# Kernel optimization log

Measured on AMD Instinct MI355X. Metric: run time of the kernel, lower is better.

The kernel has to match this reference:

```python
import jax, jax.numpy as jnp
import numpy as np

B, N, EMB, H, DH = 1, 196, 256, 8, 32
HID = 4 * EMB
EPS = 1e-5
SCALE = 16.0  # emb_size ** 0.5 (torch code scales by emb_size, not head_dim)


def _ln(x, w, b):
    m = jnp.mean(x, axis=-1, keepdims=True)
    v = jnp.mean((x - m) ** 2, axis=-1, keepdims=True)
    return (x - m) * jax.lax.rsqrt(v + EPS) * w + b


def _qkv(x, W, bias):
    # rearrange 'b n (h d qkv) -> qkv b h n d'
    t = (x @ W + bias).reshape(B, N, H, DH, 3)
    t = jnp.transpose(t, (4, 0, 2, 1, 3))
    return t[0], t[1], t[2]


def _attn(q, k, v, Wp, bp):
    att = jax.nn.softmax(jnp.einsum('bhqd,bhkd->bhqk', q, k) / SCALE, axis=-1)
    o = jnp.einsum('bhqk,bhkd->bhqd', att, v)
    o = jnp.transpose(o, (0, 2, 1, 3)).reshape(B, N, EMB)  # b n (h d)
    return o @ Wp + bp


def _ff(x, W1, b1, W2, b2):
    return jax.nn.gelu(x @ W1 + b1, approximate=False) @ W2 + b2


def _recon(x):
    x = x.reshape(B, 14, 14, 16, 16)
    x = jnp.transpose(x, (0, 3, 4, 1, 2))
    return x.reshape(B, 1, 224, 224)


def setup_inputs() -> dict:
    key = jax.random.key(0)
    ks = jax.random.split(key, 16)
    rn = lambda k, shape: jax.random.normal(k, shape, jnp.float32) * 0.02
    d = {
        'vis_emb': jax.random.normal(ks[0], (B, N, EMB), jnp.float32),
        'ir_emb': jax.random.normal(ks[1], (B, N, EMB), jnp.float32),
        'ln1v_w': jnp.ones((EMB,), jnp.float32), 'ln1v_b': jnp.zeros((EMB,), jnp.float32),
        'ln1i_w': jnp.ones((EMB,), jnp.float32), 'ln1i_b': jnp.zeros((EMB,), jnp.float32),
        'ln2v_w': jnp.ones((EMB,), jnp.float32), 'ln2v_b': jnp.zeros((EMB,), jnp.float32),
        'ln2i_w': jnp.ones((EMB,), jnp.float32), 'ln2i_b': jnp.zeros((EMB,), jnp.float32),
        'Wqkv_v': rn(ks[2], (EMB, 3 * EMB)), 'bqkv_v': jnp.zeros((3 * EMB,), jnp.float32),
        'Wqkv_i': rn(ks[3], (EMB, 3 * EMB)), 'bqkv_i': jnp.zeros((3 * EMB,), jnp.float32),
        'Wp_v': rn(ks[4], (EMB, EMB)), 'bp_v': jnp.zeros((EMB,), jnp.float32),
        'Wp_i': rn(ks[5], (EMB, EMB)), 'bp_i': jnp.zeros((EMB,), jnp.float32),
        'W1v': rn(ks[6], (EMB, HID)), 'b1v': jnp.zeros((HID,), jnp.float32),
        'W2v': rn(ks[7], (HID, EMB)), 'b2v': jnp.zeros((EMB,), jnp.float32),
        'W1i': rn(ks[8], (EMB, HID)), 'b1i': jnp.zeros((HID,), jnp.float32),
        'W2i': rn(ks[9], (HID, EMB)), 'b2i': jnp.zeros((EMB,), jnp.float32),
    }
    return d


def reference(vis_emb, ir_emb, ln1v_w, ln1v_b, ln1i_w, ln1i_b, ln2v_w, ln2v_b,
              ln2i_w, ln2i_b, Wqkv_v, bqkv_v, Wqkv_i, bqkv_i, Wp_v, bp_v,
              Wp_i, bp_i, W1v, b1v, W2v, b2v, W1i, b1i, W2i, b2i):
    nv = _ln(vis_emb, ln1v_w, ln1v_b)
    ni = _ln(ir_emb, ln1i_w, ln1i_b)
    qv, kv_, vv = _qkv(vis_emb, Wqkv_v, bqkv_v)
    qi, ki, vi = _qkv(ir_emb, Wqkv_i, bqkv_i)
    cross_v2i = _attn(qv, ki, vi, Wp_v, bp_v)   # vis queries attend ir k/v
    cross_i2v = _attn(qi, kv_, vv, Wp_i, bp_i)  # ir queries attend vis k/v
    rv = nv + cross_v2i
    ri = ni + cross_i2v
    lv = _ln(rv, ln2v_w, ln2v_b)
    li = _ln(ri, ln2i_w, ln2i_b)
    ov = _ff(lv, W1v, b1v, W2v, b2v) + lv
    oi = _ff(li, W1i, b1i, W2i, b2i) + li
    return jnp.concatenate([_recon(oi), _recon(ov)], axis=1)  # (1,2,224,224)
```

## Files before the change

kernel.cpp:

```cpp
#include <hip/hip_runtime.h>
#include <math.h>

#define NT   196
#define EMB  256
#define NH   8
#define DH   32
#define HID  1024
#define EPSV 1e-5f


__global__ __launch_bounds__(256) void k1_qkv(
    const float* __restrict__ vis, const float* __restrict__ ir,
    const float* __restrict__ Wqkv_v, const float* __restrict__ bqkv_v,
    const float* __restrict__ Wqkv_i, const float* __restrict__ bqkv_i,
    float* __restrict__ Q, float* __restrict__ Kq, float* __restrict__ Vq)
{
    const int b = blockIdx.x;
    const int s = b / 147;
    const int rem = b % 147;
    const int mt = rem / 3;
    const int cg = rem % 3;
    const int n0 = mt * 4;
    const int t = threadIdx.x;

    const float* x    = (s == 0) ? vis    : ir;
    const float* W    = (s == 0) ? Wqkv_v : Wqkv_i;
    const float* bias = (s == 0) ? bqkv_v : bqkv_i;

    __shared__ float xsT[EMB * 4];
    __shared__ float pp[4 * 4 * 256];

    {
        int r = t >> 6, c4 = (t & 63) * 4;
        float4 xv = *(const float4*)&x[(n0 + r) * EMB + c4];
        xsT[(c4 + 0) * 4 + r] = xv.x;
        xsT[(c4 + 1) * 4 + r] = xv.y;
        xsT[(c4 + 2) * 4 + r] = xv.z;
        xsT[(c4 + 3) * 4 + r] = xv.w;
    }
    __syncthreads();

    const int cq = t & 63, ks = t >> 6;
    const int col0 = cg * 256 + cq * 4;
    const float* Wb = W + col0;
    float4 a0 = {0,0,0,0}, a1 = a0, a2 = a0, a3 = a0;
    #pragma unroll 8
    for (int kk = ks * 64; kk < ks * 64 + 64; kk++) {
        float4 w4 = *(const float4*)&Wb[kk * 768];
        float4 xr = *(const float4*)&xsT[kk * 4];
        a0.x = fmaf(xr.x, w4.x, a0.x); a0.y = fmaf(xr.x, w4.y, a0.y);
        a0.z = fmaf(xr.x, w4.z, a0.z); a0.w = fmaf(xr.x, w4.w, a0.w);
        a1.x = fmaf(xr.y, w4.x, a1.x); a1.y = fmaf(xr.y, w4.y, a1.y);
        a1.z = fmaf(xr.y, w4.z, a1.z); a1.w = fmaf(xr.y, w4.w, a1.w);
        a2.x = fmaf(xr.z, w4.x, a2.x); a2.y = fmaf(xr.z, w4.y, a2.y);
        a2.z = fmaf(xr.z, w4.z, a2.z); a2.w = fmaf(xr.z, w4.w, a2.w);
        a3.x = fmaf(xr.w, w4.x, a3.x); a3.y = fmaf(xr.w, w4.y, a3.y);
        a3.z = fmaf(xr.w, w4.z, a3.z); a3.w = fmaf(xr.w, w4.w, a3.w);
    }
    *(float4*)&pp[(ks * 4 + 0) * 256 + cq * 4] = a0;
    *(float4*)&pp[(ks * 4 + 1) * 256 + cq * 4] = a1;
    *(float4*)&pp[(ks * 4 + 2) * 256 + cq * 4] = a2;
    *(float4*)&pp[(ks * 4 + 3) * 256 + cq * 4] = a3;
    __syncthreads();

    const int col = cg * 256 + t;
    const int h = col / 96, rr = col % 96, d = rr / 3, q = rr % 3;
    float* dst = (q == 0) ? Q : (q == 1 ? Kq : Vq);
    const float bval = bias[col];
    #pragma unroll
    for (int r = 0; r < 4; r++) {
        float v = pp[(0 * 4 + r) * 256 + t] + pp[(1 * 4 + r) * 256 + t]
                + pp[(2 * 4 + r) * 256 + t] + pp[(3 * 4 + r) * 256 + t] + bval;
        dst[((s * NH + h) * NT + n0 + r) * DH + d] = v;
    }
}

__global__ __launch_bounds__(256) void k2_attn(
    const float* __restrict__ Q, const float* __restrict__ Kq,
    const float* __restrict__ Vq, float* __restrict__ AO)
{
    const int b  = blockIdx.x;
    const int s  = b / 112;
    const int rm = b % 112;
    const int h  = rm / 14;
    const int rt = rm % 14;
    const int t    = threadIdx.x;
    const int wv   = t >> 6;
    const int lane = t & 63;

    __shared__ float kl[NT * 33];
    __shared__ float vl[NT * 33];
    __shared__ float pb[4][NT];

    const float4* Ks4 = (const float4*)(Kq + ((1 - s) * NH + h) * NT * DH);
    const float4* Vs4 = (const float4*)(Vq + ((1 - s) * NH + h) * NT * DH);
    for (int idx = t; idx < NT * 8; idx += 256) {
        int j = idx >> 3, d4 = (idx & 7) * 4;
        float4 kv = Ks4[idx];
        kl[j * 33 + d4 + 0] = kv.x; kl[j * 33 + d4 + 1] = kv.y;
        kl[j * 33 + d4 + 2] = kv.z; kl[j * 33 + d4 + 3] = kv.w;
        float4 vv = Vs4[idx];
        vl[j * 33 + d4 + 0] = vv.x; vl[j * 33 + d4 + 1] = vv.y;
        vl[j * 33 + d4 + 2] = vv.z; vl[j * 33 + d4 + 3] = vv.w;
    }
    __syncthreads();

    const float* Qs = Q + ((s * NH + h) * NT) * DH;
    const bool v3 = (lane + 192) < NT;
    const int  j3 = v3 ? (lane + 192) : 0;

    for (int it = 0; it < 4; it++) {
        int lr = it * 4 + wv;
        bool act = lr < 14;
        int i = rt * 14 + lr;
        float inv_sum = 0.0f;
        if (act) {
            float qreg[DH];
            #pragma unroll
            for (int d = 0; d < DH; d++) qreg[d] = Qs[i * DH + d];
            float s0 = 0.f, s1 = 0.f, s2 = 0.f, s3 = 0.f;
            #pragma unroll
            for (int d = 0; d < DH; d++) {
                float qd = qreg[d];
                s0 = fmaf(qd, kl[(lane      ) * 33 + d], s0);
                s1 = fmaf(qd, kl[(lane +  64) * 33 + d], s1);
                s2 = fmaf(qd, kl[(lane + 128) * 33 + d], s2);
                s3 = fmaf(qd, kl[ j3          * 33 + d], s3);
            }
            const float sc = 1.0f / 16.0f;
            s0 *= sc; s1 *= sc; s2 *= sc; s3 *= sc;
            float m = fmaxf(fmaxf(s0, s1), v3 ? fmaxf(s2, s3) : s2);
            #pragma unroll
            for (int mk = 32; mk >= 1; mk >>= 1) m = fmaxf(m, __shfl_xor(m, mk));
            float p0 = expf(s0 - m), p1 = expf(s1 - m), p2 = expf(s2 - m);
            float p3 = v3 ? expf(s3 - m) : 0.0f;
            float ls = p0 + p1 + p2 + p3;
            #pragma unroll
            for (int mk = 32; mk >= 1; mk >>= 1) ls += __shfl_xor(ls, mk);
            inv_sum = 1.0f / ls;
            pb[wv][lane]       = p0;
            pb[wv][lane +  64] = p1;
            pb[wv][lane + 128] = p2;
            if (v3) pb[wv][lane + 192] = p3;
        }
        __syncthreads();
        if (act) {
            int d = lane & 31, half = lane >> 5;
            float o = 0.0f;
            int jb = half * 98;
            for (int jj = 0; jj < 98; jj++) {
                int j = jb + jj;
                o = fmaf(pb[wv][j], vl[j * 33 + d], o);
            }
            o += __shfl_xor(o, 32);
            if (lane < 32) AO[(s * NT + i) * EMB + h * DH + d] = o * inv_sum;
        }
        __syncthreads();
    }
}

__global__ __launch_bounds__(256) void k3_proj_ln2(
    const float* __restrict__ vis, const float* __restrict__ ir,
    const float* __restrict__ AO,
    const float* __restrict__ ln1v_w, const float* __restrict__ ln1v_b,
    const float* __restrict__ ln1i_w, const float* __restrict__ ln1i_b,
    const float* __restrict__ Wp_v, const float* __restrict__ bp_v,
    const float* __restrict__ Wp_i, const float* __restrict__ bp_i,
    const float* __restrict__ ln2v_w, const float* __restrict__ ln2v_b,
    const float* __restrict__ ln2i_w, const float* __restrict__ ln2i_b,
    float* __restrict__ LV)
{
    const int b = blockIdx.x;
    const int s = b / 49;
    const int n0 = (b % 49) * 4;
    const int t = threadIdx.x;

    const float* x   = (s == 0) ? vis    : ir;
    const float* W   = (s == 0) ? Wp_v   : Wp_i;
    const float* bp  = (s == 0) ? bp_v   : bp_i;
    const float* l1w = (s == 0) ? ln1v_w : ln1i_w;
    const float* l1b = (s == 0) ? ln1v_b : ln1i_b;
    const float* l2w = (s == 0) ? ln2v_w : ln2i_w;
    const float* l2b = (s == 0) ? ln2v_b : ln2i_b;

    __shared__ float aoT[EMB * 4];
    __shared__ float pp[4 * 4 * 256];
    __shared__ float nvb[4 * 256];
    __shared__ float rbuf[4 * 256];

    const int r = t >> 6, lane = t & 63, c4 = lane * 4;

    {
        float4 xv = *(const float4*)&x[(n0 + r) * EMB + c4];
        float sum = xv.x + xv.y + xv.z + xv.w;
        float sq  = xv.x*xv.x + xv.y*xv.y + xv.z*xv.z + xv.w*xv.w;
        #pragma unroll
        for (int mk = 32; mk >= 1; mk >>= 1) {
            sum += __shfl_xor(sum, mk);
            sq  += __shfl_xor(sq,  mk);
        }
        float mean = sum * (1.0f / EMB);
        float inv  = rsqrtf(sq * (1.0f / EMB) - mean * mean + EPSV);
        float4 wv4 = *(const float4*)&l1w[c4];
        float4 bv4 = *(const float4*)&l1b[c4];
        nvb[r * 256 + c4 + 0] = (xv.x - mean) * inv * wv4.x + bv4.x;
        nvb[r * 256 + c4 + 1] = (xv.y - mean) * inv * wv4.y + bv4.y;
        nvb[r * 256 + c4 + 2] = (xv.z - mean) * inv * wv4.z + bv4.z;
        nvb[r * 256 + c4 + 3] = (xv.w - mean) * inv * wv4.w + bv4.w;
        float4 av = *(const float4*)&AO[(s * NT + n0 + r) * EMB + c4];
        aoT[(c4 + 0) * 4 + r] = av.x;
        aoT[(c4 + 1) * 4 + r] = av.y;
        aoT[(c4 + 2) * 4 + r] = av.z;
        aoT[(c4 + 3) * 4 + r] = av.w;
    }
    __syncthreads();

    const int cq = t & 63, ks = t >> 6;
    const int col0 = cq * 4;
    const float* Wb = W + col0;
    float4 a0 = {0,0,0,0}, a1 = a0, a2 = a0, a3 = a0;
    #pragma unroll 8
    for (int kk = ks * 64; kk < ks * 64 + 64; kk++) {
        float4 w4 = *(const float4*)&Wb[kk * EMB];
        float4 xr = *(const float4*)&aoT[kk * 4];
        a0.x = fmaf(xr.x, w4.x, a0.x); a0.y = fmaf(xr.x, w4.y, a0.y);
        a0.z = fmaf(xr.x, w4.z, a0.z); a0.w = fmaf(xr.x, w4.w, a0.w);
        a1.x = fmaf(xr.y, w4.x, a1.x); a1.y = fmaf(xr.y, w4.y, a1.y);
        a1.z = fmaf(xr.y, w4.z, a1.z); a1.w = fmaf(xr.y, w4.w, a1.w);
        a2.x = fmaf(xr.z, w4.x, a2.x); a2.y = fmaf(xr.z, w4.y, a2.y);
        a2.z = fmaf(xr.z, w4.z, a2.z); a2.w = fmaf(xr.z, w4.w, a2.w);
        a3.x = fmaf(xr.w, w4.x, a3.x); a3.y = fmaf(xr.w, w4.y, a3.y);
        a3.z = fmaf(xr.w, w4.z, a3.z); a3.w = fmaf(xr.w, w4.w, a3.w);
    }
    *(float4*)&pp[(ks * 4 + 0) * 256 + cq * 4] = a0;
    *(float4*)&pp[(ks * 4 + 1) * 256 + cq * 4] = a1;
    *(float4*)&pp[(ks * 4 + 2) * 256 + cq * 4] = a2;
    *(float4*)&pp[(ks * 4 + 3) * 256 + cq * 4] = a3;
    __syncthreads();

    {
        const float bval = bp[t];
        #pragma unroll
        for (int r2 = 0; r2 < 4; r2++) {
            float v = pp[(0 * 4 + r2) * 256 + t] + pp[(1 * 4 + r2) * 256 + t]
                    + pp[(2 * 4 + r2) * 256 + t] + pp[(3 * 4 + r2) * 256 + t]
                    + bval + nvb[r2 * 256 + t];
            rbuf[r2 * 256 + t] = v;
        }
    }
    __syncthreads();

    {
        float4 rv = *(const float4*)&rbuf[r * 256 + c4];
        float sum = rv.x + rv.y + rv.z + rv.w;
        float sq  = rv.x*rv.x + rv.y*rv.y + rv.z*rv.z + rv.w*rv.w;
        #pragma unroll
        for (int mk = 32; mk >= 1; mk >>= 1) {
            sum += __shfl_xor(sum, mk);
            sq  += __shfl_xor(sq,  mk);
        }
        float mean = sum * (1.0f / EMB);
        float inv  = rsqrtf(sq * (1.0f / EMB) - mean * mean + EPSV);
        float4 wv4 = *(const float4*)&l2w[c4];
        float4 bv4 = *(const float4*)&l2b[c4];
        float4 o;
        o.x = (rv.x - mean) * inv * wv4.x + bv4.x;
        o.y = (rv.y - mean) * inv * wv4.y + bv4.y;
        o.z = (rv.z - mean) * inv * wv4.z + bv4.z;
        o.w = (rv.w - mean) * inv * wv4.w + bv4.w;
        *(float4*)&LV[(s * NT + n0 + r) * EMB + c4] = o;
    }
}

__global__ __launch_bounds__(256) void k4_ffn1(
    const float* __restrict__ LV,
    const float* __restrict__ W1v, const float* __restrict__ b1v,
    const float* __restrict__ W1i, const float* __restrict__ b1i,
    float* __restrict__ HH)
{
    const int b = blockIdx.x;
    const int s = b / 196;
    const int rem = b % 196;
    const int mt = rem / 4;
    const int cg = rem % 4;
    const int n0 = mt * 4;
    const int t = threadIdx.x;

    const float* W  = (s == 0) ? W1v : W1i;
    const float* bb = (s == 0) ? b1v : b1i;

    __shared__ float xsT[EMB * 4];
    __shared__ float pp[4 * 4 * 256];

    {
        int r = t >> 6, c4 = (t & 63) * 4;
        float4 xv = *(const float4*)&LV[(s * NT + n0 + r) * EMB + c4];
        xsT[(c4 + 0) * 4 + r] = xv.x;
        xsT[(c4 + 1) * 4 + r] = xv.y;
        xsT[(c4 + 2) * 4 + r] = xv.z;
        xsT[(c4 + 3) * 4 + r] = xv.w;
    }
    __syncthreads();

    const int cq = t & 63, ks = t >> 6;
    const int col0 = cg * 256 + cq * 4;
    const float* Wb = W + col0;
    float4 a0 = {0,0,0,0}, a1 = a0, a2 = a0, a3 = a0;
    #pragma unroll 8
    for (int kk = ks * 64; kk < ks * 64 + 64; kk++) {
        float4 w4 = *(const float4*)&Wb[kk * HID];
        float4 xr = *(const float4*)&xsT[kk * 4];
        a0.x = fmaf(xr.x, w4.x, a0.x); a0.y = fmaf(xr.x, w4.y, a0.y);
        a0.z = fmaf(xr.x, w4.z, a0.z); a0.w = fmaf(xr.x, w4.w, a0.w);
        a1.x = fmaf(xr.y, w4.x, a1.x); a1.y = fmaf(xr.y, w4.y, a1.y);
        a1.z = fmaf(xr.y, w4.z, a1.z); a1.w = fmaf(xr.y, w4.w, a1.w);
        a2.x = fmaf(xr.z, w4.x, a2.x); a2.y = fmaf(xr.z, w4.y, a2.y);
        a2.z = fmaf(xr.z, w4.z, a2.z); a2.w = fmaf(xr.z, w4.w, a2.w);
        a3.x = fmaf(xr.w, w4.x, a3.x); a3.y = fmaf(xr.w, w4.y, a3.y);
        a3.z = fmaf(xr.w, w4.z, a3.z); a3.w = fmaf(xr.w, w4.w, a3.w);
    }
    *(float4*)&pp[(ks * 4 + 0) * 256 + cq * 4] = a0;
    *(float4*)&pp[(ks * 4 + 1) * 256 + cq * 4] = a1;
    *(float4*)&pp[(ks * 4 + 2) * 256 + cq * 4] = a2;
    *(float4*)&pp[(ks * 4 + 3) * 256 + cq * 4] = a3;
    __syncthreads();

    const int col = cg * 256 + t;
    const float bval = bb[col];
    #pragma unroll
    for (int r = 0; r < 4; r++) {
        float v = pp[(0 * 4 + r) * 256 + t] + pp[(1 * 4 + r) * 256 + t]
                + pp[(2 * 4 + r) * 256 + t] + pp[(3 * 4 + r) * 256 + t] + bval;
        float g = 0.5f * v * (1.0f + erff(v * 0.7071067811865475f));
        HH[(s * NT + n0 + r) * HID + col] = g;
    }
}

__global__ __launch_bounds__(256) void k5_ffn2_out(
    const float* __restrict__ HH, const float* __restrict__ LV,
    const float* __restrict__ W2v, const float* __restrict__ b2v,
    const float* __restrict__ W2i, const float* __restrict__ b2i,
    float* __restrict__ out)
{
    const int b = blockIdx.x;
    const int s = b / 49;
    const int n0 = (b % 49) * 4;
    const int t = threadIdx.x;

    const float* W  = (s == 0) ? W2v : W2i;
    const float* bb = (s == 0) ? b2v : b2i;

    __shared__ float hhT[HID * 4];
    __shared__ float pp[4 * 4 * 256];

    {
        int r = t >> 6, lane = t & 63;
        #pragma unroll
        for (int rd = 0; rd < 4; rd++) {
            int c4 = rd * 256 + lane * 4;
            float4 hv = *(const float4*)&HH[(s * NT + n0 + r) * HID + c4];
            hhT[(c4 + 0) * 4 + r] = hv.x;
            hhT[(c4 + 1) * 4 + r] = hv.y;
            hhT[(c4 + 2) * 4 + r] = hv.z;
            hhT[(c4 + 3) * 4 + r] = hv.w;
        }
    }
    __syncthreads();

    const int cq = t & 63, ks = t >> 6;
    const int col0 = cq * 4;
    const float* Wb = W + col0;
    float4 a0 = {0,0,0,0}, a1 = a0, a2 = a0, a3 = a0;
    #pragma unroll 8
    for (int kk = ks * 256; kk < ks * 256 + 256; kk++) {
        float4 w4 = *(const float4*)&Wb[kk * EMB];
        float4 xr = *(const float4*)&hhT[kk * 4];
        a0.x = fmaf(xr.x, w4.x, a0.x); a0.y = fmaf(xr.x, w4.y, a0.y);
        a0.z = fmaf(xr.x, w4.z, a0.z); a0.w = fmaf(xr.x, w4.w, a0.w);
        a1.x = fmaf(xr.y, w4.x, a1.x); a1.y = fmaf(xr.y, w4.y, a1.y);
        a1.z = fmaf(xr.y, w4.z, a1.z); a1.w = fmaf(xr.y, w4.w, a1.w);
        a2.x = fmaf(xr.z, w4.x, a2.x); a2.y = fmaf(xr.z, w4.y, a2.y);
        a2.z = fmaf(xr.z, w4.z, a2.z); a2.w = fmaf(xr.z, w4.w, a2.w);
        a3.x = fmaf(xr.w, w4.x, a3.x); a3.y = fmaf(xr.w, w4.y, a3.y);
        a3.z = fmaf(xr.w, w4.z, a3.z); a3.w = fmaf(xr.w, w4.w, a3.w);
    }
    *(float4*)&pp[(ks * 4 + 0) * 256 + cq * 4] = a0;
    *(float4*)&pp[(ks * 4 + 1) * 256 + cq * 4] = a1;
    *(float4*)&pp[(ks * 4 + 2) * 256 + cq * 4] = a2;
    *(float4*)&pp[(ks * 4 + 3) * 256 + cq * 4] = a3;
    __syncthreads();

    const float bval = bb[t];
    const int p1 = t >> 4, p2 = t & 15;
    const int ch = (s == 0) ? 1 : 0;
    #pragma unroll
    for (int r = 0; r < 4; r++) {
        int n = n0 + r;
        float v = pp[(0 * 4 + r) * 256 + t] + pp[(1 * 4 + r) * 256 + t]
                + pp[(2 * 4 + r) * 256 + t] + pp[(3 * 4 + r) * 256 + t]
                + bval + LV[(s * NT + n) * EMB + t];
        int n1 = n / 14, n2 = n % 14;
        int f = p1 * 3136 + p2 * 196 + n1 * 14 + n2;
        out[ch * 50176 + f] = v;
    }
}

extern "C" void kernel_launch(void* const* d_in, const int* in_sizes, int n_in,
                              void* d_out, int out_size, void* d_ws, size_t ws_size,
                              hipStream_t stream)
{
    const float* vis    = (const float*)d_in[0];
    const float* ir     = (const float*)d_in[1];
    const float* ln1v_w = (const float*)d_in[2];
    const float* ln1v_b = (const float*)d_in[3];
    const float* ln1i_w = (const float*)d_in[4];
    const float* ln1i_b = (const float*)d_in[5];
    const float* ln2v_w = (const float*)d_in[6];
    const float* ln2v_b = (const float*)d_in[7];
    const float* ln2i_w = (const float*)d_in[8];
    const float* ln2i_b = (const float*)d_in[9];
    const float* Wqkv_v = (const float*)d_in[10];
    const float* bqkv_v = (const float*)d_in[11];
    const float* Wqkv_i = (const float*)d_in[12];
    const float* bqkv_i = (const float*)d_in[13];
    const float* Wp_v   = (const float*)d_in[14];
    const float* bp_v   = (const float*)d_in[15];
    const float* Wp_i   = (const float*)d_in[16];
    const float* bp_i   = (const float*)d_in[17];
    const float* W1v    = (const float*)d_in[18];
    const float* b1v    = (const float*)d_in[19];
    const float* W2v    = (const float*)d_in[20];
    const float* b2v    = (const float*)d_in[21];
    const float* W1i    = (const float*)d_in[22];
    const float* b1i    = (const float*)d_in[23];
    const float* W2i    = (const float*)d_in[24];
    const float* b2i    = (const float*)d_in[25];

    float* ws = (float*)d_ws;
    float* Q  = ws;
    float* K  = ws + 100352;
    float* V  = ws + 200704;
    float* AO = ws + 301056;
    float* LV = ws + 401408;
    float* HH = ws + 501760;

    k1_qkv<<<294, 256, 0, stream>>>(vis, ir, Wqkv_v, bqkv_v, Wqkv_i, bqkv_i, Q, K, V);
    k2_attn<<<224, 256, 0, stream>>>(Q, K, V, AO);
    k3_proj_ln2<<<98, 256, 0, stream>>>(vis, ir, AO, ln1v_w, ln1v_b, ln1i_w, ln1i_b,
                                        Wp_v, bp_v, Wp_i, bp_i,
                                        ln2v_w, ln2v_b, ln2i_w, ln2i_b, LV);
    k4_ffn1<<<392, 256, 0, stream>>>(LV, W1v, b1v, W1i, b1i, HH);
    k5_ffn2_out<<<98, 256, 0, stream>>>(HH, LV, W2v, b2v, W2i, b2i, (float*)d_out);
}
```

Measured before the change: 170.0 us.

## Fuse five stage kernels into one cooperative persistent kernel with grid syncs

Merges the QKV, attention, projection+LN, FFN1 and FFN2 kernels into a single cooperative kernel of 256 persistent blocks. Each stage loops over its original work items and is separated from the next by grid.sync(). This removes four kernel launches and the gaps between them. In exchange it adds grid-wide barrier costs, fixes occupancy to one shared-memory footprint sized for the largest stage, and makes stages with more than 256 work items run in two waves.

```diff
diff --git a/kernel.cpp b/kernel.cpp
--- a/kernel.cpp
+++ b/kernel.cpp
@@ -1,5 +1,8 @@
 #include <hip/hip_runtime.h>
+#include <hip/hip_cooperative_groups.h>
 #include <math.h>
+
+namespace cg = cooperative_groups;
 
 #define NT   196
 #define EMB  256
@@ -8,400 +11,316 @@
 #define HID  1024
 #define EPSV 1e-5f
 
-
-__global__ __launch_bounds__(256) void k1_qkv(
-    const float* __restrict__ vis, const float* __restrict__ ir,
-    const float* __restrict__ Wqkv_v, const float* __restrict__ bqkv_v,
-    const float* __restrict__ Wqkv_i, const float* __restrict__ bqkv_i,
-    float* __restrict__ Q, float* __restrict__ Kq, float* __restrict__ Vq)
+struct Params {
+    const float *vis, *ir;
+    const float *l1vw, *l1vb, *l1iw, *l1ib;
+    const float *l2vw, *l2vb, *l2iw, *l2ib;
+    const float *Wqv, *bqv, *Wqi, *bqi;
+    const float *Wpv, *bpv, *Wpi, *bpi;
+    const float *W1v, *b1v, *W2v, *b2v;
+    const float *W1i, *b1i, *W2i, *b2i;
+    float *Q, *K, *V, *AO, *LV, *HH;
+    float *out;
+};
+
+#define GEMM_PANEL(Wptr, ldw, xsT, pp, cq, ks, KITER)                          \
+    {                                                                          \
+        const float* Wb = (Wptr);                                              \
+        float4 a0 = {0,0,0,0}, a1 = a0, a2 = a0, a3 = a0;                      \
+        _Pragma("unroll 8")                                                    \
+        for (int kk = (ks) * (KITER); kk < (ks) * (KITER) + (KITER); kk++) {   \
+            float4 w4 = *(const float4*)&Wb[kk * (ldw)];                       \
+            float4 xr = *(const float4*)&(xsT)[kk * 4];                        \
+            a0.x = fmaf(xr.x, w4.x, a0.x); a0.y = fmaf(xr.x, w4.y, a0.y);      \
+            a0.z = fmaf(xr.x, w4.z, a0.z); a0.w = fmaf(xr.x, w4.w, a0.w);      \
+            a1.x = fmaf(xr.y, w4.x, a1.x); a1.y = fmaf(xr.y, w4.y, a1.y);      \
+            a1.z = fmaf(xr.y, w4.z, a1.z); a1.w = fmaf(xr.y, w4.w, a1.w);      \
+            a2.x = fmaf(xr.z, w4.x, a2.x); a2.y = fmaf(xr.z, w4.y, a2.y);      \
+            a2.z = fmaf(xr.z, w4.z, a2.z); a2.w = fmaf(xr.z, w4.w, a2.w);      \
+            a3.x = fmaf(xr.w, w4.x, a3.x); a3.y = fmaf(xr.w, w4.y, a3.y);      \
+            a3.z = fmaf(xr.w, w4.z, a3.z); a3.w = fmaf(xr.w, w4.w, a3.w);      \
+        }                                                                      \
+        *(float4*)&(pp)[((ks) * 4 + 0) * 256 + (cq) * 4] = a0;                 \
+        *(float4*)&(pp)[((ks) * 4 + 1) * 256 + (cq) * 4] = a1;                 \
+        *(float4*)&(pp)[((ks) * 4 + 2) * 256 + (cq) * 4] = a2;                 \
+        *(float4*)&(pp)[((ks) * 4 + 3) * 256 + (cq) * 4] = a3;                 \
+    }
+
+__global__ void fused_crossvit(Params p)
 {
-    const int b = blockIdx.x;
-    const int s = b / 147;
-    const int rem = b % 147;
-    const int mt = rem / 3;
-    const int cg = rem % 3;
-    const int n0 = mt * 4;
+    cg::grid_group grid = cg::this_grid();
+    __shared__ float smem[13720];
     const int t = threadIdx.x;
 
-    const float* x    = (s == 0) ? vis    : ir;
-    const float* W    = (s == 0) ? Wqkv_v : Wqkv_i;
-    const float* bias = (s == 0) ? bqkv_v : bqkv_i;
-
-    __shared__ float xsT[EMB * 4];
-    __shared__ float pp[4 * 4 * 256];
-
-    {
-        int r = t >> 6, c4 = (t & 63) * 4;
-        float4 xv = *(const float4*)&x[(n0 + r) * EMB + c4];
-        xsT[(c4 + 0) * 4 + r] = xv.x;
-        xsT[(c4 + 1) * 4 + r] = xv.y;
-        xsT[(c4 + 2) * 4 + r] = xv.z;
-        xsT[(c4 + 3) * 4 + r] = xv.w;
-    }
-    __syncthreads();
-
-    const int cq = t & 63, ks = t >> 6;
-    const int col0 = cg * 256 + cq * 4;
-    const float* Wb = W + col0;
-    float4 a0 = {0,0,0,0}, a1 = a0, a2 = a0, a3 = a0;
-    #pragma unroll 8
-    for (int kk = ks * 64; kk < ks * 64 + 64; kk++) {
-        float4 w4 = *(const float4*)&Wb[kk * 768];
-        float4 xr = *(const float4*)&xsT[kk * 4];
-        a0.x = fmaf(xr.x, w4.x, a0.x); a0.y = fmaf(xr.x, w4.y, a0.y);
-        a0.z = fmaf(xr.x, w4.z, a0.z); a0.w = fmaf(xr.x, w4.w, a0.w);
-        a1.x = fmaf(xr.y, w4.x, a1.x); a1.y = fmaf(xr.y, w4.y, a1.y);
-        a1.z = fmaf(xr.y, w4.z, a1.z); a1.w = fmaf(xr.y, w4.w, a1.w);
-        a2.x = fmaf(xr.z, w4.x, a2.x); a2.y = fmaf(xr.z, w4.y, a2.y);
-        a2.z = fmaf(xr.z, w4.z, a2.z); a2.w = fmaf(xr.z, w4.w, a2.w);
-        a3.x = fmaf(xr.w, w4.x, a3.x); a3.y = fmaf(xr.w, w4.y, a3.y);
-        a3.z = fmaf(xr.w, w4.z, a3.z); a3.w = fmaf(xr.w, w4.w, a3.w);
-    }
-    *(float4*)&pp[(ks * 4 + 0) * 256 + cq * 4] = a0;
-    *(float4*)&pp[(ks * 4 + 1) * 256 + cq * 4] = a1;
-    *(float4*)&pp[(ks * 4 + 2) * 256 + cq * 4] = a2;
-    *(float4*)&pp[(ks * 4 + 3) * 256 + cq * 4] = a3;
-    __syncthreads();
-
-    const int col = cg * 256 + t;
-    const int h = col / 96, rr = col % 96, d = rr / 3, q = rr % 3;
-    float* dst = (q == 0) ? Q : (q == 1 ? Kq : Vq);
-    const float bval = bias[col];
-    #pragma unroll
-    for (int r = 0; r < 4; r++) {
-        float v = pp[(0 * 4 + r) * 256 + t] + pp[(1 * 4 + r) * 256 + t]
-                + pp[(2 * 4 + r) * 256 + t] + pp[(3 * 4 + r) * 256 + t] + bval;
-        dst[((s * NH + h) * NT + n0 + r) * DH + d] = v;
-    }
-}
-
-__global__ __launch_bounds__(256) void k2_attn(
-    const float* __restrict__ Q, const float* __restrict__ Kq,
-    const float* __restrict__ Vq, float* __restrict__ AO)
-{
-    const int b  = blockIdx.x;
-    const int s  = b / 112;
-    const int rm = b % 112;
-    const int h  = rm / 14;
-    const int rt = rm % 14;
-    const int t    = threadIdx.x;
-    const int wv   = t >> 6;
-    const int lane = t & 63;
-
-    __shared__ float kl[NT * 33];
-    __shared__ float vl[NT * 33];
-    __shared__ float pb[4][NT];
-
-    const float4* Ks4 = (const float4*)(Kq + ((1 - s) * NH + h) * NT * DH);
-    const float4* Vs4 = (const float4*)(Vq + ((1 - s) * NH + h) * NT * DH);
-    for (int idx = t; idx < NT * 8; idx += 256) {
-        int j = idx >> 3, d4 = (idx & 7) * 4;
-        float4 kv = Ks4[idx];
-        kl[j * 33 + d4 + 0] = kv.x; kl[j * 33 + d4 + 1] = kv.y;
-        kl[j * 33 + d4 + 2] = kv.z; kl[j * 33 + d4 + 3] = kv.w;
-        float4 vv = Vs4[idx];
-        vl[j * 33 + d4 + 0] = vv.x; vl[j * 33 + d4 + 1] = vv.y;
-        vl[j * 33 + d4 + 2] = vv.z; vl[j * 33 + d4 + 3] = vv.w;
-    }
-    __syncthreads();
-
-    const float* Qs = Q + ((s * NH + h) * NT) * DH;
-    const bool v3 = (lane + 192) < NT;
-    const int  j3 = v3 ? (lane + 192) : 0;
-
-    for (int it = 0; it < 4; it++) {
-        int lr = it * 4 + wv;
-        bool act = lr < 14;
-        int i = rt * 14 + lr;
-        float inv_sum = 0.0f;
-        if (act) {
-            float qreg[DH];
+    {
+        float* xsT = smem;
+        float* pp  = smem + 1024;
+        for (int u = blockIdx.x; u < 294; u += gridDim.x) {
+            const int s = u / 147;
+            const int rem = u % 147;
+            const int n0 = (rem / 3) * 4;
+            const int cg_ = rem % 3;
+            const float* x    = (s == 0) ? p.vis : p.ir;
+            const float* W    = (s == 0) ? p.Wqv : p.Wqi;
+            const float* bias = (s == 0) ? p.bqv : p.bqi;
+            {
+                int r = t >> 6, c4 = (t & 63) * 4;
+                float4 xv = *(const float4*)&x[(n0 + r) * EMB + c4];
+                xsT[(c4 + 0) * 4 + r] = xv.x;
+                xsT[(c4 + 1) * 4 + r] = xv.y;
+                xsT[(c4 + 2) * 4 + r] = xv.z;
+                xsT[(c4 + 3) * 4 + r] = xv.w;
+            }
+            __syncthreads();
+            const int cq = t & 63, ks = t >> 6;
+            GEMM_PANEL(W + cg_ * 256 + cq * 4, 768, xsT, pp, cq, ks, 64);
+            __syncthreads();
+            const int col = cg_ * 256 + t;
+            const int h = col / 96, rr = col % 96, d = rr / 3, q = rr % 3;
+            float* dst = (q == 0) ? p.Q : (q == 1 ? p.K : p.V);
+            const float bval = bias[col];
             #pragma unroll
-            for (int d = 0; d < DH; d++) qreg[d] = Qs[i * DH + d];
-            float s0 = 0.f, s1 = 0.f, s2 = 0.f, s3 = 0.f;
+            for (int r = 0; r < 4; r++) {
+                float v = pp[(0 * 4 + r) * 256 + t] + pp[(1 * 4 + r) * 256 + t]
+                        + pp[(2 * 4 + r) * 256 + t] + pp[(3 * 4 + r) * 256 + t] + bval;
+                dst[((s * NH + h) * NT + n0 + r) * DH + d] = v;
+            }
+            __syncthreads();
+        }
+    }
+    grid.sync();
+
+    {
+        float* kl = smem;
+        float* vl = smem + 6468;
+        float* pb = smem + 12936;
+        const int wv = t >> 6, lane = t & 63;
+        for (int u = blockIdx.x; u < 224; u += gridDim.x) {
+            const int s  = u / 112;
+            const int rm = u % 112;
+            const int h  = rm / 14;
+            const int rt = rm % 14;
+            const float4* Ks4 = (const float4*)(p.K + ((1 - s) * NH + h) * NT * DH);
+            const float4* Vs4 = (const float4*)(p.V + ((1 - s) * NH + h) * NT * DH);
+            for (int idx = t; idx < NT * 8; idx += 256) {
+                int j = idx >> 3, d4 = (idx & 7) * 4;
+                float4 kv = Ks4[idx];
+                kl[j * 33 + d4 + 0] = kv.x; kl[j * 33 + d4 + 1] = kv.y;
+                kl[j * 33 + d4 + 2] = kv.z; kl[j * 33 + d4 + 3] = kv.w;
+                float4 vv = Vs4[idx];
+                vl[j * 33 + d4 + 0] = vv.x; vl[j * 33 + d4 + 1] = vv.y;
+                vl[j * 33 + d4 + 2] = vv.z; vl[j * 33 + d4 + 3] = vv.w;
+            }
+            __syncthreads();
+            const float* Qs = p.Q + ((s * NH + h) * NT) * DH;
+            const bool v3 = (lane + 192) < NT;
+            const int  j3 = v3 ? (lane + 192) : 0;
+            for (int it = 0; it < 4; it++) {
+                int lr = it * 4 + wv;
+                bool act = lr < 14;
+                int i = rt * 14 + lr;
+                float inv_sum = 0.0f;
+                if (act) {
+                    float qreg[DH];
+                    #pragma unroll
+                    for (int d = 0; d < DH; d++) qreg[d] = Qs[i * DH + d];
+                    float s0 = 0.f, s1 = 0.f, s2 = 0.f, s3 = 0.f;
+                    #pragma unroll
+                    for (int d = 0; d < DH; d++) {
+                        float qd = qreg[d];
+                        s0 = fmaf(qd, kl[(lane      ) * 33 + d], s0);
+                        s1 = fmaf(qd, kl[(lane +  64) * 33 + d], s1);
+                        s2 = fmaf(qd, kl[(lane + 128) * 33 + d], s2);
+                        s3 = fmaf(qd, kl[ j3          * 33 + d], s3);
+                    }
+                    const float sc = 1.0f / 16.0f;
+                    s0 *= sc; s1 *= sc; s2 *= sc; s3 *= sc;
+                    float m = fmaxf(fmaxf(s0, s1), v3 ? fmaxf(s2, s3) : s2);
+                    #pragma unroll
+                    for (int mk = 32; mk >= 1; mk >>= 1) m = fmaxf(m, __shfl_xor(m, mk));
+                    float p0 = expf(s0 - m), p1 = expf(s1 - m), p2 = expf(s2 - m);
+                    float p3 = v3 ? expf(s3 - m) : 0.0f;
+                    float ls = p0 + p1 + p2 + p3;
+                    #pragma unroll
+                    for (int mk = 32; mk >= 1; mk >>= 1) ls += __shfl_xor(ls, mk);
+                    inv_sum = 1.0f / ls;
+                    pb[wv * NT + lane]       = p0;
+                    pb[wv * NT + lane +  64] = p1;
+                    pb[wv * NT + lane + 128] = p2;
+                    if (v3) pb[wv * NT + lane + 192] = p3;
+                }
+                __syncthreads();
+                if (act) {
+                    int d = lane & 31, half = lane >> 5;
+                    float o = 0.0f;
+                    int jb = half * 98;
+                    for (int jj = 0; jj < 98; jj++) {
+                        int j = jb + jj;
+                        o = fmaf(pb[wv * NT + j], vl[j * 33 + d], o);
+                    }
+                    o += __shfl_xor(o, 32);
+                    if (lane < 32) p.AO[(s * NT + i) * EMB + h * DH + d] = o * inv_sum;
+                }
+                __syncthreads();
+            }
+        }
+    }
+    grid.sync();
+
+    {
+        float* aoT  = smem;
+        float* pp   = smem + 1024;
+        float* nvb  = smem + 5120;
+        float* rbuf = smem + 6144;
+        const int r = t >> 6, lane = t & 63, c4 = lane * 4;
+        for (int u = blockIdx.x; u < 98; u += gridDim.x) {
+            const int s = u / 49;
+            const int n0 = (u % 49) * 4;
+            const float* x   = (s == 0) ? p.vis  : p.ir;
+            const float* W   = (s == 0) ? p.Wpv  : p.Wpi;
+            const float* bp  = (s == 0) ? p.bpv  : p.bpi;
+            const float* l1w = (s == 0) ? p.l1vw : p.l1iw;
+            const float* l1b = (s == 0) ? p.l1vb : p.l1ib;
+            const float* l2w = (s == 0) ? p.l2vw : p.l2iw;
+            const float* l2b = (s == 0) ? p.l2vb : p.l2ib;
+            {
+                float4 xv = *(const float4*)&x[(n0 + r) * EMB + c4];
+                float sum = xv.x + xv.y + xv.z + xv.w;
+                float sq  = xv.x*xv.x + xv.y*xv.y + xv.z*xv.z + xv.w*xv.w;
+                #pragma unroll
+                for (int mk = 32; mk >= 1; mk >>= 1) {
+                    sum += __shfl_xor(sum, mk);
+                    sq  += __shfl_xor(sq,  mk);
+                }
+                float mean = sum * (1.0f / EMB);
+                float inv  = rsqrtf(sq * (1.0f / EMB) - mean * mean + EPSV);
+                float4 wv4 = *(const float4*)&l1w[c4];
+                float4 bv4 = *(const float4*)&l1b[c4];
+                nvb[r * 256 + c4 + 0] = (xv.x - mean) * inv * wv4.x + bv4.x;
+                nvb[r * 256 + c4 + 1] = (xv.y - mean) * inv * wv4.y + bv4.y;
+                nvb[r * 256 + c4 + 2] = (xv.z - mean) * inv * wv4.z + bv4.z;
+                nvb[r * 256 + c4 + 3] = (xv.w - mean) * inv * wv4.w + bv4.w;
+                float4 av = *(const float4*)&p.AO[(s * NT + n0 + r) * EMB + c4];
+                aoT[(c4 + 0) * 4 + r] = av.x;
+                aoT[(c4 + 1) * 4 + r] = av.y;
+                aoT[(c4 + 2) * 4 + r] = av.z;
+                aoT[(c4 + 3) * 4 + r] = av.w;
+            }
+            __syncthreads();
+            const int cq = t & 63, ks = t >> 6;
+            GEMM_PANEL(W + cq * 4, EMB, aoT, pp, cq, ks, 64);
+            __syncthreads();
+            {
+                const float bval = bp[t];
+                #pragma unroll
+                for (int r2 = 0; r2 < 4; r2++) {
+                    float v = pp[(0 * 4 + r2) * 256 + t] + pp[(1 * 4 + r2) * 256 + t]
+                            + pp[(2 * 4 + r2) * 256 + t] + pp[(3 * 4 + r2) * 256 + t]
+                            + bval + nvb[r2 * 256 + t];
+                    rbuf[r2 * 256 + t] = v;
+                }
+            }
+            __syncthreads();
+            {
+                float4 rv = *(const float4*)&rbuf[r * 256 + c4];
+                float sum = rv.x + rv.y + rv.z + rv.w;
+                float sq  = rv.x*rv.x + rv.y*rv.y + rv.z*rv.z + rv.w*rv.w;
+                #pragma unroll
+                for (int mk = 32; mk >= 1; mk >>= 1) {
+                    sum += __shfl_xor(sum, mk);
+                    sq  += __shfl_xor(sq,  mk);
+                }
+                float mean = sum * (1.0f / EMB);
+                float inv  = rsqrtf(sq * (1.0f / EMB) - mean * mean + EPSV);
+                float4 wv4 = *(const float4*)&l2w[c4];
+                float4 bv4 = *(const float4*)&l2b[c4];
+                float4 o;
+                o.x = (rv.x - mean) * inv * wv4.x + bv4.x;
+                o.y = (rv.y - mean) * inv * wv4.y + bv4.y;
+                o.z = (rv.z - mean) * inv * wv4.z + bv4.z;
+                o.w = (rv.w - mean) * inv * wv4.w + bv4.w;
+                *(float4*)&p.LV[(s * NT + n0 + r) * EMB + c4] = o;
+            }
+            __syncthreads();
+        }
+    }
+    grid.sync();
+
+    {
+        float* xsT = smem;
+        float* pp  = smem + 1024;
+        for (int u = blockIdx.x; u < 392; u += gridDim.x) {
+            const int s = u / 196;
+            const int rem = u % 196;
+            const int n0 = (rem / 4) * 4;
+            const int cg_ = rem % 4;
+            const float* W  = (s == 0) ? p.W1v : p.W1i;
+            const float* bb = (s == 0) ? p.b1v : p.b1i;
+            {
+                int r = t >> 6, c4 = (t & 63) * 4;
+                float4 xv = *(const float4*)&p.LV[(s * NT + n0 + r) * EMB + c4];
+                xsT[(c4 + 0) * 4 + r] = xv.x;
+                xsT[(c4 + 1) * 4 + r] = xv.y;
+                xsT[(c4 + 2) * 4 + r] = xv.z;
+                xsT[(c4 + 3) * 4 + r] = xv.w;
+            }
+            __syncthreads();
+            const int cq = t & 63, ks = t >> 6;
+            GEMM_PANEL(W + cg_ * 256 + cq * 4, HID, xsT, pp, cq, ks, 64);
+            __syncthreads();
+            const int col = cg_ * 256 + t;
+            const float bval = bb[col];
             #pragma unroll
-            for (int d = 0; d < DH; d++) {
-                float qd = qreg[d];
-                s0 = fmaf(qd, kl[(lane      ) * 33 + d], s0);
-                s1 = fmaf(qd, kl[(lane +  64) * 33 + d], s1);
-                s2 = fmaf(qd, kl[(lane + 128) * 33 + d], s2);
-                s3 = fmaf(qd, kl[ j3          * 33 + d], s3);
-            }
-            const float sc = 1.0f / 16.0f;
-            s0 *= sc; s1 *= sc; s2 *= sc; s3 *= sc;
-            float m = fmaxf(fmaxf(s0, s1), v3 ? fmaxf(s2, s3) : s2);
+            for (int r = 0; r < 4; r++) {
+                float v = pp[(0 * 4 + r) * 256 + t] + pp[(1 * 4 + r) * 256 + t]
+                        + pp[(2 * 4 + r) * 256 + t] + pp[(3 * 4 + r) * 256 + t] + bval;
+                float g = 0.5f * v * (1.0f + erff(v * 0.7071067811865475f));
+                p.HH[(s * NT + n0 + r) * HID + col] = g;
+            }
+            __syncthreads();
+        }
+    }
+    grid.sync();
+
+    {
+        float* hhT = smem;
+        float* pp  = smem + 4096;
+        for (int u = blockIdx.x; u < 98; u += gridDim.x) {
+            const int s = u / 49;
+            const int n0 = (u % 49) * 4;
+            const float* W  = (s == 0) ? p.W2v : p.W2i;
+            const float* bb = (s == 0) ? p.b2v : p.b2i;
+            {
+                int r = t >> 6, lane = t & 63;
+                #pragma unroll
+                for (int rd = 0; rd < 4; rd++) {
+                    int c4 = rd * 256 + lane * 4;
+                    float4 hv = *(const float4*)&p.HH[(s * NT + n0 + r) * HID + c4];
+                    hhT[(c4 + 0) * 4 + r] = hv.x;
+                    hhT[(c4 + 1) * 4 + r] = hv.y;
+                    hhT[(c4 + 2) * 4 + r] = hv.z;
+                    hhT[(c4 + 3) * 4 + r] = hv.w;
+                }
+            }
+            __syncthreads();
+            const int cq = t & 63, ks = t >> 6;
+            GEMM_PANEL(W + cq * 4, EMB, hhT, pp, cq, ks, 256);
+            __syncthreads();
+            const float bval = bb[t];
+            const int p1 = t >> 4, p2 = t & 15;
+            const int ch = (s == 0) ? 1 : 0;
             #pragma unroll
-            for (int mk = 32; mk >= 1; mk >>= 1) m = fmaxf(m, __shfl_xor(m, mk));
-            float p0 = expf(s0 - m), p1 = expf(s1 - m), p2 = expf(s2 - m);
-            float p3 = v3 ? expf(s3 - m) : 0.0f;
-            float ls = p0 + p1 + p2 + p3;
-            #pragma unroll
-            for (int mk = 32; mk >= 1; mk >>= 1) ls += __shfl_xor(ls, mk);
-            inv_sum = 1.0f / ls;
-            pb[wv][lane]       = p0;
-            pb[wv][lane +  64] = p1;
-            pb[wv][lane + 128] = p2;
-            if (v3) pb[wv][lane + 192] = p3;
-        }
-        __syncthreads();
-        if (act) {
-            int d = lane & 31, half = lane >> 5;
-            float o = 0.0f;
-            int jb = half * 98;
-            for (int jj = 0; jj < 98; jj++) {
-                int j = jb + jj;
-                o = fmaf(pb[wv][j], vl[j * 33 + d], o);
-            }
-            o += __shfl_xor(o, 32);
-            if (lane < 32) AO[(s * NT + i) * EMB + h * DH + d] = o * inv_sum;
-        }
-        __syncthreads();
-    }
-}
-
-__global__ __launch_bounds__(256) void k3_proj_ln2(
-    const float* __restrict__ vis, const float* __restrict__ ir,
-    const float* __restrict__ AO,
-    const float* __restrict__ ln1v_w, const float* __restrict__ ln1v_b,
-    const float* __restrict__ ln1i_w, const float* __restrict__ ln1i_b,
-    const float* __restrict__ Wp_v, const float* __restrict__ bp_v,
-    const float* __restrict__ Wp_i, const float* __restrict__ bp_i,
-    const float* __restrict__ ln2v_w, const float* __restrict__ ln2v_b,
-    const float* __restrict__ ln2i_w, const float* __restrict__ ln2i_b,
-    float* __restrict__ LV)
-{
-    const int b = blockIdx.x;
-    const int s = b / 49;
-    const int n0 = (b % 49) * 4;
-    const int t = threadIdx.x;
-
-    const float* x   = (s == 0) ? vis    : ir;
-    const float* W   = (s == 0) ? Wp_v   : Wp_i;
-    const float* bp  = (s == 0) ? bp_v   : bp_i;
-    const float* l1w = (s == 0) ? ln1v_w : ln1i_w;
-    const float* l1b = (s == 0) ? ln1v_b : ln1i_b;
-    const float* l2w = (s == 0) ? ln2v_w : ln2i_w;
-    const float* l2b = (s == 0) ? ln2v_b : ln2i_b;
-
-    __shared__ float aoT[EMB * 4];
-    __shared__ float pp[4 * 4 * 256];
-    __shared__ float nvb[4 * 256];
-    __shared__ float rbuf[4 * 256];
-
-    const int r = t >> 6, lane = t & 63, c4 = lane * 4;
-
-    {
-        float4 xv = *(const float4*)&x[(n0 + r) * EMB + c4];
-        float sum = xv.x + xv.y + xv.z + xv.w;
-        float sq  = xv.x*xv.x + xv.y*xv.y + xv.z*xv.z + xv.w*xv.w;
-        #pragma unroll
-        for (int mk = 32; mk >= 1; mk >>= 1) {
-            sum += __shfl_xor(sum, mk);
-            sq  += __shfl_xor(sq,  mk);
-        }
-        float mean = sum * (1.0f / EMB);
-        float inv  = rsqrtf(sq * (1.0f / EMB) - mean * mean + EPSV);
-        float4 wv4 = *(const float4*)&l1w[c4];
-        float4 bv4 = *(const float4*)&l1b[c4];
-        nvb[r * 256 + c4 + 0] = (xv.x - mean) * inv * wv4.x + bv4.x;
-        nvb[r * 256 + c4 + 1] = (xv.y - mean) * inv * wv4.y + bv4.y;
-        nvb[r * 256 + c4 + 2] = (xv.z - mean) * inv * wv4.z + bv4.z;
-        nvb[r * 256 + c4 + 3] = (xv.w - mean) * inv * wv4.w + bv4.w;
-        float4 av = *(const float4*)&AO[(s * NT + n0 + r) * EMB + c4];
-        aoT[(c4 + 0) * 4 + r] = av.x;
-        aoT[(c4 + 1) * 4 + r] = av.y;
-        aoT[(c4 + 2) * 4 + r] = av.z;
-        aoT[(c4 + 3) * 4 + r] = av.w;
-    }
-    __syncthreads();
-
-    const int cq = t & 63, ks = t >> 6;
-    const int col0 = cq * 4;
-    const float* Wb = W + col0;
-    float4 a0 = {0,0,0,0}, a1 = a0, a2 = a0, a3 = a0;
-    #pragma unroll 8
-    for (int kk = ks * 64; kk < ks * 64 + 64; kk++) {
-        float4 w4 = *(const float4*)&Wb[kk * EMB];
-        float4 xr = *(const float4*)&aoT[kk * 4];
-        a0.x = fmaf(xr.x, w4.x, a0.x); a0.y = fmaf(xr.x, w4.y, a0.y);
-        a0.z = fmaf(xr.x, w4.z, a0.z); a0.w = fmaf(xr.x, w4.w, a0.w);
-        a1.x = fmaf(xr.y, w4.x, a1.x); a1.y = fmaf(xr.y, w4.y, a1.y);
-        a1.z = fmaf(xr.y, w4.z, a1.z); a1.w = fmaf(xr.y, w4.w, a1.w);
-        a2.x = fmaf(xr.z, w4.x, a2.x); a2.y = fmaf(xr.z, w4.y, a2.y);
-        a2.z = fmaf(xr.z, w4.z, a2.z); a2.w = fmaf(xr.z, w4.w, a2.w);
-        a3.x = fmaf(xr.w, w4.x, a3.x); a3.y = fmaf(xr.w, w4.y, a3.y);
-        a3.z = fmaf(xr.w, w4.z, a3.z); a3.w = fmaf(xr.w, w4.w, a3.w);
-    }
-    *(float4*)&pp[(ks * 4 + 0) * 256 + cq * 4] = a0;
-    *(float4*)&pp[(ks * 4 + 1) * 256 + cq * 4] = a1;
-    *(float4*)&pp[(ks * 4 + 2) * 256 + cq * 4] = a2;
-    *(float4*)&pp[(ks * 4 + 3) * 256 + cq * 4] = a3;
-    __syncthreads();
-
-    {
-        const float bval = bp[t];
-        #pragma unroll
-        for (int r2 = 0; r2 < 4; r2++) {
-            float v = pp[(0 * 4 + r2) * 256 + t] + pp[(1 * 4 + r2) * 256 + t]
-                    + pp[(2 * 4 + r2) * 256 + t] + pp[(3 * 4 + r2) * 256 + t]
-                    + bval + nvb[r2 * 256 + t];
-            rbuf[r2 * 256 + t] = v;
-        }
-    }
-    __syncthreads();
-
-    {
-        float4 rv = *(const float4*)&rbuf[r * 256 + c4];
-        float sum = rv.x + rv.y + rv.z + rv.w;
-        float sq  = rv.x*rv.x + rv.y*rv.y + rv.z*rv.z + rv.w*rv.w;
-        #pragma unroll
-        for (int mk = 32; mk >= 1; mk >>= 1) {
-            sum += __shfl_xor(sum, mk);
-            sq  += __shfl_xor(sq,  mk);
-        }
-        float mean = sum * (1.0f / EMB);
-        float inv  = rsqrtf(sq * (1.0f / EMB) - mean * mean + EPSV);
-        float4 wv4 = *(const float4*)&l2w[c4];
-        float4 bv4 = *(const float4*)&l2b[c4];
-        float4 o;
-        o.x = (rv.x - mean) * inv * wv4.x + bv4.x;
-        o.y = (rv.y - mean) * inv * wv4.y + bv4.y;
-        o.z = (rv.z - mean) * inv * wv4.z + bv4.z;
-        o.w = (rv.w - mean) * inv * wv4.w + bv4.w;
-        *(float4*)&LV[(s * NT + n0 + r) * EMB + c4] = o;
-    }
-}
-
-__global__ __launch_bounds__(256) void k4_ffn1(
-    const float* __restrict__ LV,
-    const float* __restrict__ W1v, const float* __restrict__ b1v,
-    const float* __restrict__ W1i, const float* __restrict__ b1i,
-    float* __restrict__ HH)
-{
-    const int b = blockIdx.x;
-    const int s = b / 196;
-    const int rem = b % 196;
-    const int mt = rem / 4;
-    const int cg = rem % 4;
-    const int n0 = mt * 4;
-    const int t = threadIdx.x;
-
-    const float* W  = (s == 0) ? W1v : W1i;
-    const float* bb = (s == 0) ? b1v : b1i;
-
-    __shared__ float xsT[EMB * 4];
-    __shared__ float pp[4 * 4 * 256];
-
-    {
-        int r = t >> 6, c4 = (t & 63) * 4;
-        float4 xv = *(const float4*)&LV[(s * NT + n0 + r) * EMB + c4];
-        xsT[(c4 + 0) * 4 + r] = xv.x;
-        xsT[(c4 + 1) * 4 + r] = xv.y;
-        xsT[(c4 + 2) * 4 + r] = xv.z;
-        xsT[(c4 + 3) * 4 + r] = xv.w;
-    }
-    __syncthreads();
-
-    const int cq = t & 63, ks = t >> 6;
-    const int col0 = cg * 256 + cq * 4;
-    const float* Wb = W + col0;
-    float4 a0 = {0,0,0,0}, a1 = a0, a2 = a0, a3 = a0;
-    #pragma unroll 8
-    for (int kk = ks * 64; kk < ks * 64 + 64; kk++) {
-        float4 w4 = *(const float4*)&Wb[kk * HID];
-        float4 xr = *(const float4*)&xsT[kk * 4];
-        a0.x = fmaf(xr.x, w4.x, a0.x); a0.y = fmaf(xr.x, w4.y, a0.y);
-        a0.z = fmaf(xr.x, w4.z, a0.z); a0.w = fmaf(xr.x, w4.w, a0.w);
-        a1.x = fmaf(xr.y, w4.x, a1.x); a1.y = fmaf(xr.y, w4.y, a1.y);
-        a1.z = fmaf(xr.y, w4.z, a1.z); a1.w = fmaf(xr.y, w4.w, a1.w);
-        a2.x = fmaf(xr.z, w4.x, a2.x); a2.y = fmaf(xr.z, w4.y, a2.y);
-        a2.z = fmaf(xr.z, w4.z, a2.z); a2.w = fmaf(xr.z, w4.w, a2.w);
-        a3.x = fmaf(xr.w, w4.x, a3.x); a3.y = fmaf(xr.w, w4.y, a3.y);
-        a3.z = fmaf(xr.w, w4.z, a3.z); a3.w = fmaf(xr.w, w4.w, a3.w);
-    }
-    *(float4*)&pp[(ks * 4 + 0) * 256 + cq * 4] = a0;
-    *(float4*)&pp[(ks * 4 + 1) * 256 + cq * 4] = a1;
-    *(float4*)&pp[(ks * 4 + 2) * 256 + cq * 4] = a2;
-    *(float4*)&pp[(ks * 4 + 3) * 256 + cq * 4] = a3;
-    __syncthreads();
-
-    const int col = cg * 256 + t;
-    const float bval = bb[col];
-    #pragma unroll
-    for (int r = 0; r < 4; r++) {
-        float v = pp[(0 * 4 + r) * 256 + t] + pp[(1 * 4 + r) * 256 + t]
-                + pp[(2 * 4 + r) * 256 + t] + pp[(3 * 4 + r) * 256 + t] + bval;
-        float g = 0.5f * v * (1.0f + erff(v * 0.7071067811865475f));
-        HH[(s * NT + n0 + r) * HID + col] = g;
-    }
-}
-
-__global__ __launch_bounds__(256) void k5_ffn2_out(
-    const float* __restrict__ HH, const float* __restrict__ LV,
-    const float* __restrict__ W2v, const float* __restrict__ b2v,
-    const float* __restrict__ W2i, const float* __restrict__ b2i,
-    float* __restrict__ out)
-{
-    const int b = blockIdx.x;
-    const int s = b / 49;
-    const int n0 = (b % 49) * 4;
-    const int t = threadIdx.x;
-
-    const float* W  = (s == 0) ? W2v : W2i;
-    const float* bb = (s == 0) ? b2v : b2i;
-
-    __shared__ float hhT[HID * 4];
-    __shared__ float pp[4 * 4 * 256];
-
-    {
-        int r = t >> 6, lane = t & 63;
-        #pragma unroll
-        for (int rd = 0; rd < 4; rd++) {
-            int c4 = rd * 256 + lane * 4;
-            float4 hv = *(const float4*)&HH[(s * NT + n0 + r) * HID + c4];
-            hhT[(c4 + 0) * 4 + r] = hv.x;
-            hhT[(c4 + 1) * 4 + r] = hv.y;
-            hhT[(c4 + 2) * 4 + r] = hv.z;
-            hhT[(c4 + 3) * 4 + r] = hv.w;
-        }
-    }
-    __syncthreads();
-
-    const int cq = t & 63, ks = t >> 6;
-    const int col0 = cq * 4;
-    const float* Wb = W + col0;
-    float4 a0 = {0,0,0,0}, a1 = a0, a2 = a0, a3 = a0;
-    #pragma unroll 8
-    for (int kk = ks * 256; kk < ks * 256 + 256; kk++) {
-        float4 w4 = *(const float4*)&Wb[kk * EMB];
-        float4 xr = *(const float4*)&hhT[kk * 4];
-        a0.x = fmaf(xr.x, w4.x, a0.x); a0.y = fmaf(xr.x, w4.y, a0.y);
-        a0.z = fmaf(xr.x, w4.z, a0.z); a0.w = fmaf(xr.x, w4.w, a0.w);
-        a1.x = fmaf(xr.y, w4.x, a1.x); a1.y = fmaf(xr.y, w4.y, a1.y);
-        a1.z = fmaf(xr.y, w4.z, a1.z); a1.w = fmaf(xr.y, w4.w, a1.w);
-        a2.x = fmaf(xr.z, w4.x, a2.x); a2.y = fmaf(xr.z, w4.y, a2.y);
-        a2.z = fmaf(xr.z, w4.z, a2.z); a2.w = fmaf(xr.z, w4.w, a2.w);
-        a3.x = fmaf(xr.w, w4.x, a3.x); a3.y = fmaf(xr.w, w4.y, a3.y);
-        a3.z = fmaf(xr.w, w4.z, a3.z); a3.w = fmaf(xr.w, w4.w, a3.w);
-    }
-    *(float4*)&pp[(ks * 4 + 0) * 256 + cq * 4] = a0;
-    *(float4*)&pp[(ks * 4 + 1) * 256 + cq * 4] = a1;
-    *(float4*)&pp[(ks * 4 + 2) * 256 + cq * 4] = a2;
-    *(float4*)&pp[(ks * 4 + 3) * 256 + cq * 4] = a3;
-    __syncthreads();
-
-    const float bval = bb[t];
-    const int p1 = t >> 4, p2 = t & 15;
-    const int ch = (s == 0) ? 1 : 0;
-    #pragma unroll
-    for (int r = 0; r < 4; r++) {
-        int n = n0 + r;
-        float v = pp[(0 * 4 + r) * 256 + t] + pp[(1 * 4 + r) * 256 + t]
-                + pp[(2 * 4 + r) * 256 + t] + pp[(3 * 4 + r) * 256 + t]
-                + bval + LV[(s * NT + n) * EMB + t];
-        int n1 = n / 14, n2 = n % 14;
-        int f = p1 * 3136 + p2 * 196 + n1 * 14 + n2;
-        out[ch * 50176 + f] = v;
+            for (int r = 0; r < 4; r++) {
+                int n = n0 + r;
+                float v = pp[(0 * 4 + r) * 256 + t] + pp[(1 * 4 + r) * 256 + t]
+                        + pp[(2 * 4 + r) * 256 + t] + pp[(3 * 4 + r) * 256 + t]
+                        + bval + p.LV[(s * NT + n) * EMB + t];
+                int n1 = n / 14, n2 = n % 14;
+                int f = p1 * 3136 + p2 * 196 + n1 * 14 + n2;
+                p.out[ch * 50176 + f] = v;
+            }
+            __syncthreads();
+        }
     }
 }
 
@@ -409,46 +328,44 @@
                               void* d_out, int out_size, void* d_ws, size_t ws_size,
                               hipStream_t stream)
 {
-    const float* vis    = (const float*)d_in[0];
-    const float* ir     = (const float*)d_in[1];
-    const float* ln1v_w = (const float*)d_in[2];
-    const float* ln1v_b = (const float*)d_in[3];
-    const float* ln1i_w = (const float*)d_in[4];
-    const float* ln1i_b = (const float*)d_in[5];
-    const float* ln2v_w = (const float*)d_in[6];
-    const float* ln2v_b = (const float*)d_in[7];
-    const float* ln2i_w = (const float*)d_in[8];
-    const float* ln2i_b = (const float*)d_in[9];
-    const float* Wqkv_v = (const float*)d_in[10];
-    const float* bqkv_v = (const float*)d_in[11];
-    const float* Wqkv_i = (const float*)d_in[12];
-    const float* bqkv_i = (const float*)d_in[13];
-    const float* Wp_v   = (const float*)d_in[14];
-    const float* bp_v   = (const float*)d_in[15];
-    const float* Wp_i   = (const float*)d_in[16];
-    const float* bp_i   = (const float*)d_in[17];
-    const float* W1v    = (const float*)d_in[18];
-    const float* b1v    = (const float*)d_in[19];
-    const float* W2v    = (const float*)d_in[20];
-    const float* b2v    = (const float*)d_in[21];
-    const float* W1i    = (const float*)d_in[22];
-    const float* b1i    = (const float*)d_in[23];
-    const float* W2i    = (const float*)d_in[24];
-    const float* b2i    = (const float*)d_in[25];
+    Params p;
+    p.vis  = (const float*)d_in[0];
+    p.ir   = (const float*)d_in[1];
+    p.l1vw = (const float*)d_in[2];
+    p.l1vb = (const float*)d_in[3];
+    p.l1iw = (const float*)d_in[4];
+    p.l1ib = (const float*)d_in[5];
+    p.l2vw = (const float*)d_in[6];
+    p.l2vb = (const float*)d_in[7];
+    p.l2iw = (const float*)d_in[8];
+    p.l2ib = (const float*)d_in[9];
+    p.Wqv  = (const float*)d_in[10];
+    p.bqv  = (const float*)d_in[11];
+    p.Wqi  = (const float*)d_in[12];
+    p.bqi  = (const float*)d_in[13];
+    p.Wpv  = (const float*)d_in[14];
+    p.bpv  = (const float*)d_in[15];
+    p.Wpi  = (const float*)d_in[16];
+    p.bpi  = (const float*)d_in[17];
+    p.W1v  = (const float*)d_in[18];
+    p.b1v  = (const float*)d_in[19];
+    p.W2v  = (const float*)d_in[20];
+    p.b2v  = (const float*)d_in[21];
+    p.W1i  = (const float*)d_in[22];
+    p.b1i  = (const float*)d_in[23];
+    p.W2i  = (const float*)d_in[24];
+    p.b2i  = (const float*)d_in[25];
 
     float* ws = (float*)d_ws;
-    float* Q  = ws;
-    float* K  = ws + 100352;
-    float* V  = ws + 200704;
-    float* AO = ws + 301056;
-    float* LV = ws + 401408;
-    float* HH = ws + 501760;
-
-    k1_qkv<<<294, 256, 0, stream>>>(vis, ir, Wqkv_v, bqkv_v, Wqkv_i, bqkv_i, Q, K, V);
-    k2_attn<<<224, 256, 0, stream>>>(Q, K, V, AO);
-    k3_proj_ln2<<<98, 256, 0, stream>>>(vis, ir, AO, ln1v_w, ln1v_b, ln1i_w, ln1i_b,
-                                        Wp_v, bp_v, Wp_i, bp_i,
-                                        ln2v_w, ln2v_b, ln2i_w, ln2i_b, LV);
-    k4_ffn1<<<392, 256, 0, stream>>>(LV, W1v, b1v, W1i, b1i, HH);
-    k5_ffn2_out<<<98, 256, 0, stream>>>(HH, LV, W2v, b2v, W2i, b2i, (float*)d_out);
+    p.Q  = ws;
+    p.K  = ws + 100352;
+    p.V  = ws + 200704;
+    p.AO = ws + 301056;
+    p.LV = ws + 401408;
+    p.HH = ws + 501760;
+    p.out = (float*)d_out;
+
+    void* args[] = { &p };
+    hipLaunchCooperativeKernel((void*)fused_crossvit, dim3(256), dim3(256),
+                               args, 0, stream);
 }
```

New measurement: 305.2 us. 79.6% more time.
